# Kernel optimization log

Measured on AMD Instinct MI355X. Metric: run time of the kernel, lower is better.

Reference implementation:

```python
import jax, jax.numpy as jnp
import numpy as np

KSIZE = 8
STRIDE = 4
HEADS = 8
DIM_HEAD = 32
EPS = 1e-5


def _layernorm(x, g, b):
    m = jnp.mean(x, axis=-1, keepdims=True)
    v = jnp.mean(jnp.square(x - m), axis=-1, keepdims=True)
    return (x - m) / jnp.sqrt(v + EPS) * g + b


def setup_inputs() -> dict:
    key = jax.random.key(0)
    ks = jax.random.split(key, 4)
    B, H, W, C = 8, 64, 64, 256
    inner = HEADS * DIM_HEAD  # 256
    x = jax.random.normal(ks[0], (B, H, W, C), dtype=jnp.float32)
    return {
        "x": x,
        "ln1_g": jnp.ones((C,), jnp.float32),
        "ln1_b": jnp.zeros((C,), jnp.float32),
        "ln2_g": jnp.ones((C,), jnp.float32),
        "ln2_b": jnp.zeros((C,), jnp.float32),
        "w_qkv": jax.random.normal(ks[1], (C, inner * 3), jnp.float32) * 0.02,
        "w_out": jax.random.normal(ks[2], (inner, C), jnp.float32) * 0.02,
        "b_out": jnp.zeros((C,), jnp.float32),
    }


def reference(x, ln1_g, ln1_b, ln2_g, ln2_b, w_qkv, w_out, b_out):
    B, H, W, C = x.shape
    k, s = KSIZE, STRIDE
    nH = (H - k) // s + 1
    nW = (W - k) // s + 1
    L = nH * nW
    n = k * k  # tokens per window

    # window index grids (im2col / unfold)
    rows = jnp.arange(nH)[:, None] * s + jnp.arange(k)[None, :]  # [nH, k]
    cols = jnp.arange(nW)[:, None] * s + jnp.arange(k)[None, :]  # [nW, k]
    ridx = rows[:, None, :, None]  # [nH,1,k,1]
    cidx = cols[None, :, None, :]  # [1,nW,1,k]

    # unfold: [B, nH, nW, k, k, C] -> [(B L), (k k), C]
    patches = x[:, ridx, cidx, :].reshape(B * L, n, C)

    # LocalAttention2D.norm then AttentionBlock.norm
    p = _layernorm(patches, ln1_g, ln1_b)
    h = _layernorm(p, ln2_g, ln2_b)

    qkv = h @ w_qkv  # [(B L), n, 3*inner]
    q, kk, v = jnp.split(qkv, 3, axis=-1)
    q = q.reshape(B * L, n, HEADS, DIM_HEAD)
    kk = kk.reshape(B * L, n, HEADS, DIM_HEAD)
    v = v.reshape(B * L, n, HEADS, DIM_HEAD)

    scale = DIM_HEAD ** -0.5
    dots = jnp.einsum('bnhd,bmhd->bhnm', q, kk) * scale
    attn = jax.nn.softmax(dots, axis=-1)
    o = jnp.einsum('bhnm,bmhd->bnhd', attn, v).reshape(B * L, n, HEADS * DIM_HEAD)
    o = o @ w_out + b_out  # [(B L), n, C]

    # fold (col2im overlap-add)
    o = o.reshape(B, nH, nW, k, k, C)
    out = jnp.zeros((B, H, W, C), x.dtype).at[:, ridx, cidx, :].add(o)

    # normalization: fold(unfold(ones)) == overlap counts
    counts = jnp.zeros((H, W), x.dtype).at[ridx, cidx].add(1.0)
    return out / counts[None, :, :, None]
```

## Files before the change

### kernel.cpp

```cpp
#include <hip/hip_runtime.h>
#include <hip/hip_bf16.h>
#include <cstdint>
#include <cstddef>

#define LN_EPS 1e-5f
#define B_    8
#define HW_   64
#define C_    256
#define NTOK  (B_ * HW_ * HW_)
#define HEADS_ 8
#define DH_    32

__global__ __launch_bounds__(256) void ln_stats_kernel(
    const float* __restrict__ x, const float* __restrict__ g1,
    const float* __restrict__ b1, float4* __restrict__ stats)
{
    const int gid  = blockIdx.x * 256 + threadIdx.x;
    const int tok  = gid >> 6;
    const int lane = gid & 63;
    if (tok >= NTOK) return;
    const float4 xv = reinterpret_cast<const float4*>(x + (size_t)tok * C_)[lane];
    float s  = xv.x + xv.y + xv.z + xv.w;
    float sq = xv.x*xv.x + xv.y*xv.y + xv.z*xv.z + xv.w*xv.w;
    for (int off = 32; off; off >>= 1) {
        s  += __shfl_xor(s, off);
        sq += __shfl_xor(sq, off);
    }
    const float m1 = s * (1.0f / 256.0f);
    const float r1 = rsqrtf(fmaxf(sq * (1.0f / 256.0f) - m1 * m1, 0.0f) + LN_EPS);
    const float4 g = reinterpret_cast<const float4*>(g1)[lane];
    const float4 b = reinterpret_cast<const float4*>(b1)[lane];
    const float y0 = (xv.x - m1) * r1 * g.x + b.x;
    const float y1 = (xv.y - m1) * r1 * g.y + b.y;
    const float y2 = (xv.z - m1) * r1 * g.z + b.z;
    const float y3 = (xv.w - m1) * r1 * g.w + b.w;
    float s2  = y0 + y1 + y2 + y3;
    float sq2 = y0*y0 + y1*y1 + y2*y2 + y3*y3;
    for (int off = 32; off; off >>= 1) {
        s2  += __shfl_xor(s2, off);
        sq2 += __shfl_xor(sq2, off);
    }
    const float m2 = s2 * (1.0f / 256.0f);
    const float r2 = rsqrtf(fmaxf(sq2 * (1.0f / 256.0f) - m2 * m2, 0.0f) + LN_EPS);
    if (lane == 0) stats[tok] = make_float4(m1, r1, m2, r2);
}

__global__ __launch_bounds__(256) void qkv_kernel(
    const float* __restrict__ x, const float4* __restrict__ stats,
    const float* __restrict__ g1, const float* __restrict__ b1,
    const float* __restrict__ g2, const float* __restrict__ b2,
    const float* __restrict__ w, float* __restrict__ qkv)
{
    __shared__ float At[32][130];
    __shared__ float Bt[32][132];
    const int tid  = threadIdx.x;
    const int tok0 = blockIdx.y * 128;
    const int n0   = blockIdx.x * 128;
    const int ty = tid >> 4, tx = tid & 15;
    const int ar  = tid >> 1;
    const int asb = (tid & 1) * 4;

    const float4 s4 = stats[tok0 + ar];
    const float m1 = s4.x, r1 = s4.y, m2 = s4.z, r2 = s4.w;
    const float* xrow = x + (size_t)(tok0 + ar) * C_;

    float acc[8][8] = {};

    for (int it = 0; it < 8; ++it) {
        const int k0 = it * 32;
        float4 av[4];
        #pragma unroll
        for (int u = 0; u < 4; ++u) {
            const int ka = k0 + (asb + u) * 4;
            const float4 xv  = *reinterpret_cast<const float4*>(xrow + ka);
            const float4 g1v = *reinterpret_cast<const float4*>(g1 + ka);
            const float4 b1v = *reinterpret_cast<const float4*>(b1 + ka);
            const float4 g2v = *reinterpret_cast<const float4*>(g2 + ka);
            const float4 b2v = *reinterpret_cast<const float4*>(b2 + ka);
            av[u].x = ((xv.x - m1) * r1 * g1v.x + b1v.x - m2) * r2 * g2v.x + b2v.x;
            av[u].y = ((xv.y - m1) * r1 * g1v.y + b1v.y - m2) * r2 * g2v.y + b2v.y;
            av[u].z = ((xv.z - m1) * r1 * g1v.z + b1v.z - m2) * r2 * g2v.z + b2v.z;
            av[u].w = ((xv.w - m1) * r1 * g1v.w + b1v.w - m2) * r2 * g2v.w + b2v.w;
        }
        float4 bv[4];
        #pragma unroll
        for (int rep = 0; rep < 4; ++rep) {
            const int e  = rep * 256 + tid;
            const int bk = e >> 5, bc = (e & 31) * 4;
            bv[rep] = *reinterpret_cast<const float4*>(w + (size_t)(k0 + bk) * 768 + n0 + bc);
        }
        __syncthreads();
        #pragma unroll
        for (int u = 0; u < 4; ++u) {
            const int kk = (asb + u) * 4;
            At[kk + 0][ar] = av[u].x;
            At[kk + 1][ar] = av[u].y;
            At[kk + 2][ar] = av[u].z;
            At[kk + 3][ar] = av[u].w;
        }
        #pragma unroll
        for (int rep = 0; rep < 4; ++rep) {
            const int e  = rep * 256 + tid;
            const int bk = e >> 5, bc = (e & 31) * 4;
            *reinterpret_cast<float4*>(&Bt[bk][bc]) = bv[rep];
        }
        __syncthreads();
        #pragma unroll
        for (int k = 0; k < 32; ++k) {
            const float4 a0 = *reinterpret_cast<const float4*>(&At[k][ty*8]);
            const float4 a1 = *reinterpret_cast<const float4*>(&At[k][ty*8 + 4]);
            const float4 b0 = *reinterpret_cast<const float4*>(&Bt[k][tx*4]);
            const float4 b1 = *reinterpret_cast<const float4*>(&Bt[k][64 + tx*4]);
            const float a[8] = {a0.x, a0.y, a0.z, a0.w, a1.x, a1.y, a1.z, a1.w};
            const float b[8] = {b0.x, b0.y, b0.z, b0.w, b1.x, b1.y, b1.z, b1.w};
            #pragma unroll
            for (int i = 0; i < 8; ++i) {
                #pragma unroll
                for (int j = 0; j < 8; ++j)
                    acc[i][j] = fmaf(a[i], b[j], acc[i][j]);
            }
        }
    }
    #pragma unroll
    for (int i = 0; i < 8; ++i) {
        float* orow = qkv + (size_t)(tok0 + ty*8 + i) * 768 + n0;
        *reinterpret_cast<float4*>(orow + tx*4) =
            make_float4(acc[i][0], acc[i][1], acc[i][2], acc[i][3]);
        *reinterpret_cast<float4*>(orow + 64 + tx*4) =
            make_float4(acc[i][4], acc[i][5], acc[i][6], acc[i][7]);
    }
}

__global__ __launch_bounds__(256) void attn_kernel(
    const float* __restrict__ qkv, float* __restrict__ out,
    int gi, int gj, int nJ)
{
    __shared__ float q_lds[64][36];
    __shared__ float k_lds[64][36];
    __shared__ float v_lds[64][36];
    __shared__ float p_lds[64][68];
    const int tid = threadIdx.x;
    const int b  = blockIdx.y;
    const int hd = blockIdx.z;
    const int pi = 2 * (blockIdx.x / nJ) + gi;
    const int pj = 2 * (blockIdx.x % nJ) + gj;
    const int t = tid >> 2, seg = tid & 3;
    const int pr = t >> 3, pc = t & 7;
    const size_t pixbase = ((size_t)((b * 64 + 4*pi + pr) * 64) + (4*pj + pc));
    {
        const size_t base = pixbase * 768 + hd * 32 + seg * 8;
        const float4 qa = *reinterpret_cast<const float4*>(qkv + base);
        const float4 qb = *reinterpret_cast<const float4*>(qkv + base + 4);
        const float4 ka = *reinterpret_cast<const float4*>(qkv + base + 256);
        const float4 kb = *reinterpret_cast<const float4*>(qkv + base + 260);
        const float4 va = *reinterpret_cast<const float4*>(qkv + base + 512);
        const float4 vb = *reinterpret_cast<const float4*>(qkv + base + 516);
        *reinterpret_cast<float4*>(&q_lds[t][seg*8    ]) = qa;
        *reinterpret_cast<float4*>(&q_lds[t][seg*8 + 4]) = qb;
        *reinterpret_cast<float4*>(&k_lds[t][seg*8    ]) = ka;
        *reinterpret_cast<float4*>(&k_lds[t][seg*8 + 4]) = kb;
        *reinterpret_cast<float4*>(&v_lds[t][seg*8    ]) = va;
        *reinterpret_cast<float4*>(&v_lds[t][seg*8 + 4]) = vb;
    }
    __syncthreads();
    const float scale = 0.17677669529663687f;
    float4 q4[8];
    #pragma unroll
    for (int u = 0; u < 8; ++u) q4[u] = *reinterpret_cast<const float4*>(&q_lds[t][u*4]);
    float p[16];
    #pragma unroll
    for (int jj = 0; jj < 16; ++jj) {
        const int jc = seg + jj * 4;
        float a0 = 0.f, a1 = 0.f, a2 = 0.f, a3 = 0.f;
        #pragma unroll
        for (int u = 0; u < 8; ++u) {
            const float4 kv = *reinterpret_cast<const float4*>(&k_lds[jc][u*4]);
            a0 = fmaf(q4[u].x, kv.x, a0);
            a1 = fmaf(q4[u].y, kv.y, a1);
            a2 = fmaf(q4[u].z, kv.z, a2);
            a3 = fmaf(q4[u].w, kv.w, a3);
        }
        p[jj] = ((a0 + a1) + (a2 + a3)) * scale;
    }
    float m = p[0];
    #pragma unroll
    for (int jj = 1; jj < 16; ++jj) m = fmaxf(m, p[jj]);
    m = fmaxf(m, __shfl_xor(m, 1));
    m = fmaxf(m, __shfl_xor(m, 2));
    float s = 0.f;
    #pragma unroll
    for (int jj = 0; jj < 16; ++jj) { p[jj] = __expf(p[jj] - m); s += p[jj]; }
    s += __shfl_xor(s, 1);
    s += __shfl_xor(s, 2);
    const float rs = 1.0f / s;
    #pragma unroll
    for (int jj = 0; jj < 16; ++jj) p_lds[t][seg + jj*4] = p[jj] * rs;
    __syncthreads();
    float4 o0 = make_float4(0,0,0,0), o1 = make_float4(0,0,0,0);
    for (int jc = 0; jc < 64; ++jc) {
        const float a = p_lds[t][jc];
        const float4 v0 = *reinterpret_cast<const float4*>(&v_lds[jc][seg*8]);
        const float4 v1 = *reinterpret_cast<const float4*>(&v_lds[jc][seg*8 + 4]);
        o0.x = fmaf(a, v0.x, o0.x); o0.y = fmaf(a, v0.y, o0.y);
        o0.z = fmaf(a, v0.z, o0.z); o0.w = fmaf(a, v0.w, o0.w);
        o1.x = fmaf(a, v1.x, o1.x); o1.y = fmaf(a, v1.y, o1.y);
        o1.z = fmaf(a, v1.z, o1.z); o1.w = fmaf(a, v1.w, o1.w);
    }
    float* op = out + pixbase * 256 + hd * 32 + seg * 8;
    float4 c0 = *reinterpret_cast<const float4*>(op);
    float4 c1 = *reinterpret_cast<const float4*>(op + 4);
    c0.x += o0.x; c0.y += o0.y; c0.z += o0.z; c0.w += o0.w;
    c1.x += o1.x; c1.y += o1.y; c1.z += o1.z; c1.w += o1.w;
    *reinterpret_cast<float4*>(op)     = c0;
    *reinterpret_cast<float4*>(op + 4) = c1;
}

__global__ __launch_bounds__(256) void proj_kernel(
    float* __restrict__ out, const float* __restrict__ w, const float* __restrict__ bo)
{
    __shared__ float At[16][36];
    __shared__ float Bt[16][256];
    const int tid  = threadIdx.x;
    const int tok0 = blockIdx.x * 32;
    const int ty = tid >> 5, tx = tid & 31;
    const int st = tid >> 2, sseg = tid & 3;
    const int bc = (tid & 63) * 4, bkb = tid >> 6;
    float ascale = 0.f;
    if (tid < 128) {
        const int token = tok0 + st;
        const int hp = (token >> 6) & 63, wp = token & 63;
        const float cnt = ((hp >= 4 && hp < 60) ? 2.f : 1.f) * ((wp >= 4 && wp < 60) ? 2.f : 1.f);
        ascale = 1.0f / cnt;
    }
    float acc[4][8] = {};
    for (int kk = 0; kk < 16; ++kk) {
        const int k0 = kk * 16;
        float4 av = make_float4(0,0,0,0);
        if (tid < 128)
            av = *reinterpret_cast<const float4*>(out + (size_t)(tok0 + st) * 256 + k0 + sseg * 4);
        float4 wv[4];
        #pragma unroll
        for (int u = 0; u < 4; ++u)
            wv[u] = *reinterpret_cast<const float4*>(w + (size_t)(k0 + bkb*4 + u) * 256 + bc);
        __syncthreads();
        if (tid < 128) {
            At[sseg*4+0][st] = av.x * ascale;
            At[sseg*4+1][st] = av.y * ascale;
            At[sseg*4+2][st] = av.z * ascale;
            At[sseg*4+3][st] = av.w * ascale;
        }
        #pragma unroll
        for (int u = 0; u < 4; ++u)
            *reinterpret_cast<float4*>(&Bt[bkb*4+u][bc]) = wv[u];
        __syncthreads();
        #pragma unroll
        for (int k = 0; k < 16; ++k) {
            const float4 a  = *reinterpret_cast<const float4*>(&At[k][ty*4]);
            const float4 b0 = *reinterpret_cast<const float4*>(&Bt[k][tx*4]);
            const float4 b1 = *reinterpret_cast<const float4*>(&Bt[k][128 + tx*4]);
            acc[0][0] += a.x*b0.x; acc[0][1] += a.x*b0.y; acc[0][2] += a.x*b0.z; acc[0][3] += a.x*b0.w;
            acc[0][4] += a.x*b1.x; acc[0][5] += a.x*b1.y; acc[0][6] += a.x*b1.z; acc[0][7] += a.x*b1.w;
            acc[1][0] += a.y*b0.x; acc[1][1] += a.y*b0.y; acc[1][2] += a.y*b0.z; acc[1][3] += a.y*b0.w;
            acc[1][4] += a.y*b1.x; acc[1][5] += a.y*b1.y; acc[1][6] += a.y*b1.z; acc[1][7] += a.y*b1.w;
            acc[2][0] += a.z*b0.x; acc[2][1] += a.z*b0.y; acc[2][2] += a.z*b0.z; acc[2][3] += a.z*b0.w;
            acc[2][4] += a.z*b1.x; acc[2][5] += a.z*b1.y; acc[2][6] += a.z*b1.z; acc[2][7] += a.z*b1.w;
            acc[3][0] += a.w*b0.x; acc[3][1] += a.w*b0.y; acc[3][2] += a.w*b0.z; acc[3][3] += a.w*b0.w;
            acc[3][4] += a.w*b1.x; acc[3][5] += a.w*b1.y; acc[3][6] += a.w*b1.z; acc[3][7] += a.w*b1.w;
        }
    }
    const float4 bo0 = *reinterpret_cast<const float4*>(bo + tx*4);
    const float4 bo1 = *reinterpret_cast<const float4*>(bo + 128 + tx*4);
    #pragma unroll
    for (int r = 0; r < 4; ++r) {
        float* orow = out + (size_t)(tok0 + ty*4 + r) * 256;
        const float4 o0 = make_float4(acc[r][0]+bo0.x, acc[r][1]+bo0.y, acc[r][2]+bo0.z, acc[r][3]+bo0.w);
        const float4 o1 = make_float4(acc[r][4]+bo1.x, acc[r][5]+bo1.y, acc[r][6]+bo1.z, acc[r][7]+bo1.w);
        *reinterpret_cast<float4*>(orow + tx*4)       = o0;
        *reinterpret_cast<float4*>(orow + 128 + tx*4) = o1;
    }
}

extern "C" void kernel_launch(void* const* d_in, const int* in_sizes, int n_in,
                              void* d_out, int out_size, void* d_ws, size_t ws_size,
                              hipStream_t stream)
{
    const float* x     = (const float*)d_in[0];
    const float* ln1_g = (const float*)d_in[1];
    const float* ln1_b = (const float*)d_in[2];
    const float* ln2_g = (const float*)d_in[3];
    const float* ln2_b = (const float*)d_in[4];
    const float* w_qkv = (const float*)d_in[5];
    const float* w_out = (const float*)d_in[6];
    const float* b_out = (const float*)d_in[7];
    float* out = (float*)d_out;
    float* ws  = (float*)d_ws;

    float4* stats = (float4*)ws;
    float*  qkv   = ws + (size_t)NTOK * 4;

    ln_stats_kernel<<<NTOK / 4, 256, 0, stream>>>(x, ln1_g, ln1_b, stats);
    qkv_kernel<<<dim3(6, NTOK / 128), 256, 0, stream>>>(
        x, stats, ln1_g, ln1_b, ln2_g, ln2_b, w_qkv, qkv);
    hipMemsetAsync(d_out, 0, (size_t)out_size * sizeof(float), stream);
    for (int g = 0; g < 4; ++g) {
        const int gi = g >> 1, gj = g & 1;
        const int nI = gi ? 7 : 8, nJ = gj ? 7 : 8;
        attn_kernel<<<dim3(nI * nJ, B_, HEADS_), 256, 0, stream>>>(qkv, out, gi, gj, nJ);
    }
    proj_kernel<<<NTOK / 32, 256, 0, stream>>>(out, w_out, b_out);
}
```

Baseline: 465.2 us.

## Prefetch QKV GEMM tiles, fold layernorm affine algebra, drop output memset

The QKV GEMM now loads the next k-tile's x and weight values into registers while computing on the current tile, so global latency overlaps with the FMA loop. The two chained layernorms are folded into per-row scalars plus per-channel vectors precomputed in shared memory, which removes four per-iteration global gamma/beta loads. The first attention window group stores its result directly instead of reading and adding, which lets the output memset be dropped. That relies on the first group (even window rows and columns) covering every pixel, and it adds register pressure from the prefetch buffers.

```diff
diff --git a/kernel.cpp b/kernel.cpp
--- a/kernel.cpp
+++ b/kernel.cpp
@@ -53,6 +53,7 @@
 {
     __shared__ float At[32][130];
     __shared__ float Bt[32][132];
+    __shared__ float u_lds[4][256];
     const int tid  = threadIdx.x;
     const int tok0 = blockIdx.y * 128;
     const int n0   = blockIdx.x * 128;
@@ -60,43 +61,52 @@
     const int ar  = tid >> 1;
     const int asb = (tid & 1) * 4;
 
+    {
+        const float g2v = g2[tid];
+        u_lds[0][tid] = g1[tid] * g2v;
+        u_lds[1][tid] = g2v * b1[tid];
+        u_lds[2][tid] = g2v;
+        u_lds[3][tid] = b2[tid];
+    }
+
     const float4 s4 = stats[tok0 + ar];
-    const float m1 = s4.x, r1 = s4.y, m2 = s4.z, r2 = s4.w;
+    const float alpha = s4.y * s4.w;
+    const float beta  = s4.w;
+    const float gamma = s4.z * s4.w;
+    const float delta = s4.x * s4.y * s4.w;
     const float* xrow = x + (size_t)(tok0 + ar) * C_;
 
     float acc[8][8] = {};
-
-    for (int it = 0; it < 8; ++it) {
+    float4 av[4];
+    float4 bv[4];
+
+    auto load_tiles = [&](const int it) {
         const int k0 = it * 32;
-        float4 av[4];
-        #pragma unroll
-        for (int u = 0; u < 4; ++u) {
-            const int ka = k0 + (asb + u) * 4;
-            const float4 xv  = *reinterpret_cast<const float4*>(xrow + ka);
-            const float4 g1v = *reinterpret_cast<const float4*>(g1 + ka);
-            const float4 b1v = *reinterpret_cast<const float4*>(b1 + ka);
-            const float4 g2v = *reinterpret_cast<const float4*>(g2 + ka);
-            const float4 b2v = *reinterpret_cast<const float4*>(b2 + ka);
-            av[u].x = ((xv.x - m1) * r1 * g1v.x + b1v.x - m2) * r2 * g2v.x + b2v.x;
-            av[u].y = ((xv.y - m1) * r1 * g1v.y + b1v.y - m2) * r2 * g2v.y + b2v.y;
-            av[u].z = ((xv.z - m1) * r1 * g1v.z + b1v.z - m2) * r2 * g2v.z + b2v.z;
-            av[u].w = ((xv.w - m1) * r1 * g1v.w + b1v.w - m2) * r2 * g2v.w + b2v.w;
-        }
-        float4 bv[4];
+        #pragma unroll
+        for (int u = 0; u < 4; ++u)
+            av[u] = *reinterpret_cast<const float4*>(xrow + k0 + (asb + u) * 4);
         #pragma unroll
         for (int rep = 0; rep < 4; ++rep) {
             const int e  = rep * 256 + tid;
             const int bk = e >> 5, bc = (e & 31) * 4;
             bv[rep] = *reinterpret_cast<const float4*>(w + (size_t)(k0 + bk) * 768 + n0 + bc);
         }
-        __syncthreads();
+    };
+
+    auto write_tiles = [&](const int it) {
+        const int k0 = it * 32;
         #pragma unroll
         for (int u = 0; u < 4; ++u) {
+            const int ka = k0 + (asb + u) * 4;
             const int kk = (asb + u) * 4;
-            At[kk + 0][ar] = av[u].x;
-            At[kk + 1][ar] = av[u].y;
-            At[kk + 2][ar] = av[u].z;
-            At[kk + 3][ar] = av[u].w;
+            const float4 u1 = *reinterpret_cast<const float4*>(&u_lds[0][ka & 255]);
+            const float4 u2 = *reinterpret_cast<const float4*>(&u_lds[1][ka & 255]);
+            const float4 u3 = *reinterpret_cast<const float4*>(&u_lds[2][ka & 255]);
+            const float4 u4 = *reinterpret_cast<const float4*>(&u_lds[3][ka & 255]);
+            At[kk + 0][ar] = fmaf(u1.x, fmaf(alpha, av[u].x, -delta), fmaf(beta, u2.x, fmaf(-gamma, u3.x, u4.x)));
+            At[kk + 1][ar] = fmaf(u1.y, fmaf(alpha, av[u].y, -delta), fmaf(beta, u2.y, fmaf(-gamma, u3.y, u4.y)));
+            At[kk + 2][ar] = fmaf(u1.z, fmaf(alpha, av[u].z, -delta), fmaf(beta, u2.z, fmaf(-gamma, u3.z, u4.z)));
+            At[kk + 3][ar] = fmaf(u1.w, fmaf(alpha, av[u].w, -delta), fmaf(beta, u2.w, fmaf(-gamma, u3.w, u4.w)));
         }
         #pragma unroll
         for (int rep = 0; rep < 4; ++rep) {
@@ -104,7 +114,14 @@
             const int bk = e >> 5, bc = (e & 31) * 4;
             *reinterpret_cast<float4*>(&Bt[bk][bc]) = bv[rep];
         }
+    };
+
+    load_tiles(0);
+    for (int it = 0; it < 8; ++it) {
         __syncthreads();
+        write_tiles(it);
+        __syncthreads();
+        if (it < 7) load_tiles(it + 1);
         #pragma unroll
         for (int k = 0; k < 32; ++k) {
             const float4 a0 = *reinterpret_cast<const float4*>(&At[k][ty*8]);
@@ -133,7 +150,7 @@
 
 __global__ __launch_bounds__(256) void attn_kernel(
     const float* __restrict__ qkv, float* __restrict__ out,
-    int gi, int gj, int nJ)
+    int gi, int gj, int nJ, int do_store)
 {
     __shared__ float q_lds[64][36];
     __shared__ float k_lds[64][36];
@@ -207,12 +224,17 @@
         o1.z = fmaf(a, v1.z, o1.z); o1.w = fmaf(a, v1.w, o1.w);
     }
     float* op = out + pixbase * 256 + hd * 32 + seg * 8;
-    float4 c0 = *reinterpret_cast<const float4*>(op);
-    float4 c1 = *reinterpret_cast<const float4*>(op + 4);
-    c0.x += o0.x; c0.y += o0.y; c0.z += o0.z; c0.w += o0.w;
-    c1.x += o1.x; c1.y += o1.y; c1.z += o1.z; c1.w += o1.w;
-    *reinterpret_cast<float4*>(op)     = c0;
-    *reinterpret_cast<float4*>(op + 4) = c1;
+    if (do_store) {
+        *reinterpret_cast<float4*>(op)     = o0;
+        *reinterpret_cast<float4*>(op + 4) = o1;
+    } else {
+        float4 c0 = *reinterpret_cast<const float4*>(op);
+        float4 c1 = *reinterpret_cast<const float4*>(op + 4);
+        c0.x += o0.x; c0.y += o0.y; c0.z += o0.z; c0.w += o0.w;
+        c1.x += o1.x; c1.y += o1.y; c1.z += o1.z; c1.w += o1.w;
+        *reinterpret_cast<float4*>(op)     = c0;
+        *reinterpret_cast<float4*>(op + 4) = c1;
+    }
 }
 
 __global__ __launch_bounds__(256) void proj_kernel(
@@ -301,11 +323,11 @@
     ln_stats_kernel<<<NTOK / 4, 256, 0, stream>>>(x, ln1_g, ln1_b, stats);
     qkv_kernel<<<dim3(6, NTOK / 128), 256, 0, stream>>>(
         x, stats, ln1_g, ln1_b, ln2_g, ln2_b, w_qkv, qkv);
-    hipMemsetAsync(d_out, 0, (size_t)out_size * sizeof(float), stream);
     for (int g = 0; g < 4; ++g) {
         const int gi = g >> 1, gj = g & 1;
         const int nI = gi ? 7 : 8, nJ = gj ? 7 : 8;
-        attn_kernel<<<dim3(nI * nJ, B_, HEADS_), 256, 0, stream>>>(qkv, out, gi, gj, nJ);
+        attn_kernel<<<dim3(nI * nJ, B_, HEADS_), 256, 0, stream>>>(
+            qkv, out, gi, gj, nJ, (g == 0) ? 1 : 0);
     }
     proj_kernel<<<NTOK / 32, 256, 0, stream>>>(out, w_out, b_out);
 }
```

Measured after the change: 502.5 us. 8.0% more time.
